# Kernel optimization log

Hardware: AMD Instinct MI355X
Metric: run time of the kernel (lower is better)

## Reference

```python
import jax, jax.numpy as jnp
import numpy as np

T, D, H = 10, 45, 45  # time steps, input features, hidden size (hard-coded in source)


def _lstm_step(x, h, c, W_ih, W_hh, b_ih, b_hh):
    # PyTorch nn.LSTM single step; gate order i, f, g, o
    gates = x @ W_ih.T + b_ih + h @ W_hh.T + b_hh
    i, f, g, o = jnp.split(gates, 4, axis=-1)
    c2 = jax.nn.sigmoid(f) * c + jax.nn.sigmoid(i) * jnp.tanh(g)
    h2 = jax.nn.sigmoid(o) * jnp.tanh(c2)
    return h2, c2


def setup_inputs() -> dict:
    key = jax.random.key(0)
    ks = jax.random.split(key, 20)
    s = 0.1
    return {
        "price_input": jax.random.normal(ks[0], (T, D), dtype=jnp.float32),
        # encoder input attention: Linear(2H+T -> 1)
        "Wa": jax.random.normal(ks[1], (1, 2 * H + T), dtype=jnp.float32) * s,
        "ba": jax.random.normal(ks[2], (1,), dtype=jnp.float32) * s,
        # encoder LSTM
        "Wih_e": jax.random.normal(ks[3], (4 * H, D), dtype=jnp.float32) * s,
        "Whh_e": jax.random.normal(ks[4], (4 * H, H), dtype=jnp.float32) * s,
        "bih_e": jax.random.normal(ks[5], (4 * H,), dtype=jnp.float32) * s,
        "bhh_e": jax.random.normal(ks[6], (4 * H,), dtype=jnp.float32) * s,
        # decoder temporal attention: Linear(2H+D -> D), Tanh, Linear(D -> 1)
        "W1": jax.random.normal(ks[7], (D, 2 * H + D), dtype=jnp.float32) * s,
        "b1": jax.random.normal(ks[8], (D,), dtype=jnp.float32) * s,
        "W2": jax.random.normal(ks[9], (1, D), dtype=jnp.float32) * s,
        "b2": jax.random.normal(ks[10], (1,), dtype=jnp.float32) * s,
        # decoder LSTM (input dim = D)
        "Wih_d": jax.random.normal(ks[11], (4 * H, D), dtype=jnp.float32) * s,
        "Whh_d": jax.random.normal(ks[12], (4 * H, H), dtype=jnp.float32) * s,
        "bih_d": jax.random.normal(ks[13], (4 * H,), dtype=jnp.float32) * s,
        "bhh_d": jax.random.normal(ks[14], (4 * H,), dtype=jnp.float32) * s,
        # final fc: Linear(2H -> predict_size=45)
        "Wfc": jax.random.normal(ks[15], (45, 2 * H), dtype=jnp.float32) * s,
        "bfc": jax.random.normal(ks[16], (45,), dtype=jnp.float32) * s,
    }


def reference(price_input, Wa, ba, Wih_e, Whh_e, bih_e, bhh_e,
              W1, b1, W2, b2, Wih_d, Whh_d, bih_d, bhh_d, Wfc, bfc):
    x = price_input[None]                      # [1, T, D]
    xT = jnp.transpose(x, (0, 2, 1))           # [1, D, T]

    def enc_step(carry, x_t):
        h, c = carry                           # each [1, H]
        hr = jnp.broadcast_to(h[:, None, :], (1, D, H))
        cr = jnp.broadcast_to(c[:, None, :], (1, D, H))
        feat = jnp.concatenate([hr, cr, xT], axis=2)      # [1, D, 2H+T]
        scores = (feat @ Wa.T + ba)[..., 0]               # [1, D]
        attn = jax.nn.softmax(scores, axis=-1)            # over input features
        wi = attn * x_t[None]                             # [1, D]
        h2, c2 = _lstm_step(wi, h, c, Wih_e, Whh_e, bih_e, bhh_e)
        return (h2, c2), h2

    z = jnp.zeros((1, H), dtype=price_input.dtype)
    (_, _), hs = jax.lax.scan(enc_step, (z, z), price_input)
    price_vec = jnp.transpose(hs, (1, 0, 2))              # [1, T, H]

    # decoder: temporal attention over the T encoder states (hidden=cell=0)
    h0 = jnp.zeros((1, H), dtype=price_input.dtype)
    c0 = h0
    hr = jnp.broadcast_to(h0[:, None, :], (1, T, H))
    feat = jnp.concatenate([hr, hr, price_vec], axis=2)   # [1, T, 2H+D]
    scores = (jnp.tanh(feat @ W1.T + b1) @ W2.T + b2)[..., 0]  # [1, T]
    attn = jax.nn.softmax(scores, axis=-1)
    context = jnp.einsum('bt,bth->bh', attn, price_vec)   # [1, H]

    h1, _ = _lstm_step(context, h0, c0, Wih_d, Whh_d, bih_d, bhh_d)
    y_pred = jnp.concatenate([h1, context], axis=1) @ Wfc.T + bfc  # [1, 45]
    return y_pred
```

## Files before the change

kernel.cpp:

```cpp
#include <hip/hip_runtime.h>


static constexpr int NT = 10;
static constexpr int ND = 45;
static constexpr int NH = 45;
static constexpr int NG = 4 * NH;

__device__ __forceinline__ float rcp_(float x) { return __builtin_amdgcn_rcpf(x); }
__device__ __forceinline__ float sigf(float x) { return rcp_(1.0f + __expf(-x)); }
__device__ __forceinline__ float tanh_(float x) { return 1.0f - 2.0f * rcp_(1.0f + __expf(2.0f * x)); }

__global__ __launch_bounds__(256) void darnn_kernel(
    const float* __restrict__ X,
    const float* __restrict__ Wa,
    const float* __restrict__ Wih_e,
    const float* __restrict__ Whh_e,
    const float* __restrict__ bih_e,
    const float* __restrict__ bhh_e,
    const float* __restrict__ W1,
    const float* __restrict__ b1,
    const float* __restrict__ W2,
    const float* __restrict__ Wih_d,
    const float* __restrict__ bih_d,
    const float* __restrict__ bhh_d,
    const float* __restrict__ Wfc,
    const float* __restrict__ bfc,
    float* __restrict__ out)
{
    const int tid  = threadIdx.x;
    const int wave = tid >> 6;
    const int lane = tid & 63;
    const int g    = tid - 64;

    __shared__ float sX[NT * ND];
    __shared__ float sattn[ND];
    __shared__ float sWi[NT * ND];
    __shared__ float sGx[NT * NG];
    __shared__ float shs[NT * NH];
    __shared__ float sW1c[ND * ND];
    __shared__ float sWfc[45 * 2 * NH];
    __shared__ float sb1[ND];
    __shared__ float sW2v[ND];
    __shared__ float sbfcv[45];
    __shared__ float sat[NT];
    __shared__ float sctx[NH];
    __shared__ float sh1v[NH];
    __shared__ float sg[NG];
    __shared__ float sdec[NT * NH];

    float w0[45], w1[45], w2[45], w3[45];
    float we[45], wd[45];
    float be = 0.0f, bd = 0.0f;
    if (wave == 0) {
        const int j = (lane < 45) ? lane : 0;
        const float* r0 = Whh_e + (j)       * NH;
        const float* r1 = Whh_e + (45 + j)  * NH;
        const float* r2 = Whh_e + (90 + j)  * NH;
        const float* r3 = Whh_e + (135 + j) * NH;
#pragma unroll
        for (int k = 0; k < 45; ++k) {
            w0[k] = r0[k]; w1[k] = r1[k]; w2[k] = r2[k]; w3[k] = r3[k];
        }
    } else {
        if (g < NG) {
            const float* wrE = Wih_e + g * ND;
            const float* wrD = Wih_d + g * ND;
#pragma unroll
            for (int d = 0; d < 45; ++d) { we[d] = wrE[d]; wd[d] = wrD[d]; }
            be = bih_e[g] + bhh_e[g];
            bd = bih_d[g] + bhh_d[g];
        }
        if (wave >= 2)
            for (int i = tid - 128; i < NT * ND; i += 128) sX[i] = X[i];
    }
    __syncthreads();

    if (wave == 1) {
        float acc = -1e30f;
        if (lane < ND) {
            acc = 0.0f;
            for (int t = 0; t < NT; ++t) acc += Wa[90 + t] * sX[t * ND + lane];
        }
        float m = acc;
        for (int off = 32; off; off >>= 1) m = fmaxf(m, __shfl_xor(m, off, 64));
        float e = (lane < ND) ? __expf(acc - m) : 0.0f;
        float s = e;
        for (int off = 32; off; off >>= 1) s += __shfl_xor(s, off, 64);
        if (lane < ND) sattn[lane] = e * rcp_(s);
        __builtin_amdgcn_s_waitcnt(0);
        __builtin_amdgcn_wave_barrier();
        for (int i = lane; i < NT * ND; i += 64) sWi[i] = sattn[i % ND] * sX[i];
    }
    __syncthreads();

    if (wave > 0 && g < NG) {
        float acc[NT];
#pragma unroll
        for (int t = 0; t < NT; ++t) acc[t] = be;
        for (int d = 0; d < ND; ++d) {
            const float wv = we[d];
#pragma unroll
            for (int t = 0; t < NT; ++t) acc[t] += wv * sWi[t * ND + d];
        }
#pragma unroll
        for (int t = 0; t < NT; ++t) sGx[t * NG + g] = acc[t];
    }
    __syncthreads();

    if (wave == 0) {
        const int j = (lane < 45) ? lane : 0;
        float h = 0.0f, c = 0.0f;
        for (int t = 0; t < NT; ++t) {
            float a0 = sGx[t * NG + j];
            float a1 = sGx[t * NG + 45 + j];
            float a2 = sGx[t * NG + 90 + j];
            float a3 = sGx[t * NG + 135 + j];
#pragma unroll
            for (int k = 0; k < 45; ++k) {
                const float hk = __shfl(h, k, 64);
                a0 += w0[k] * hk; a1 += w1[k] * hk;
                a2 += w2[k] * hk; a3 += w3[k] * hk;
            }
            c = sigf(a1) * c + sigf(a0) * tanh_(a2);
            h = sigf(a3) * tanh_(c);
            if (lane < 45) shs[t * NH + lane] = h;
        }
    } else {
        const int i0 = tid - 64;
        {
            const float2* s2 = (const float2*)Wfc;
            float2* d2 = (float2*)sWfc;
            for (int i = i0; i < 2025; i += 192) d2[i] = s2[i];
        }
        for (int i = i0; i < ND * ND; i += 192) {
            const int r = i / 45, cc = i - r * 45;
            sW1c[i] = W1[r * 135 + 90 + cc];
        }
        if (i0 < 45) { sb1[i0] = b1[i0]; sW2v[i0] = W2[i0]; sbfcv[i0] = bfc[i0]; }
    }
    __syncthreads();

    for (int i = tid; i < NT * NH; i += 256) {
        const int t = i / NH, k = i - t * NH;
        const float* wr = sW1c + k * ND;
        const float* hv = shs + t * NH;
        float a = sb1[k];
        for (int jj = 0; jj < ND; ++jj) a += wr[jj] * hv[jj];
        sdec[i] = sW2v[k] * tanh_(a);
    }
    __syncthreads();

    if (tid < NT) {
        float a = 0.0f;
        for (int k = 0; k < NH; ++k) a += sdec[tid * NH + k];
        sat[tid] = a;
    }
    __syncthreads();
    if (tid == 0) {
        float m = -1e30f;
        for (int t = 0; t < NT; ++t) m = fmaxf(m, sat[t]);
        float e[NT], s = 0.0f;
        for (int t = 0; t < NT; ++t) { e[t] = __expf(sat[t] - m); s += e[t]; }
        const float inv = rcp_(s);
        for (int t = 0; t < NT; ++t) sat[t] = e[t] * inv;
    }
    __syncthreads();

    if (tid < NH) {
        float a = 0.0f;
        for (int t = 0; t < NT; ++t) a += sat[t] * shs[t * NH + tid];
        sctx[tid] = a;
    }
    __syncthreads();

    if (wave > 0 && g < NG) {
        float a = bd;
#pragma unroll
        for (int d = 0; d < 45; ++d) a += wd[d] * sctx[d];
        sg[g] = a;
    }
    __syncthreads();
    if (tid < NH) {
        const float ig = sigf(sg[tid]);
        const float gg = tanh_(sg[2 * NH + tid]);
        const float og = sigf(sg[3 * NH + tid]);
        sh1v[tid] = og * tanh_(ig * gg);
    }
    __syncthreads();

    if (tid < 45) {
        const float* wr = sWfc + tid * (2 * NH);
        float a = sbfcv[tid];
        for (int jj = 0; jj < NH; ++jj) a += wr[jj] * sh1v[jj];
        for (int jj = 0; jj < NH; ++jj) a += wr[NH + jj] * sctx[jj];
        out[tid] = a;
    }
}

extern "C" void kernel_launch(void* const* d_in, const int* in_sizes, int n_in,
                              void* d_out, int out_size, void* d_ws, size_t ws_size,
                              hipStream_t stream) {
    const float* X     = (const float*)d_in[0];
    const float* Wa    = (const float*)d_in[1];
    const float* Wih_e = (const float*)d_in[3];
    const float* Whh_e = (const float*)d_in[4];
    const float* bih_e = (const float*)d_in[5];
    const float* bhh_e = (const float*)d_in[6];
    const float* W1    = (const float*)d_in[7];
    const float* b1    = (const float*)d_in[8];
    const float* W2    = (const float*)d_in[9];
    const float* Wih_d = (const float*)d_in[11];
    const float* bih_d = (const float*)d_in[13];
    const float* bhh_d = (const float*)d_in[14];
    const float* Wfc   = (const float*)d_in[15];
    const float* bfc   = (const float*)d_in[16];
    float* out = (float*)d_out;

    darnn_kernel<<<dim3(1), dim3(256), 0, stream>>>(
        X, Wa, Wih_e, Whh_e, bih_e, bhh_e, W1, b1, W2,
        Wih_d, bih_d, bhh_d, Wfc, bfc, out);
}
```

Before: 105.6 us.

## Stage recurrent and input weights through shared memory with coalesced float4 loads

Weight loading changes from strided per-thread row reads from global memory to coalesced float4 copies. Whh_e is staged into a shared buffer that the recurrent wave then reads into registers. Wih_e is held in registers as float4s and written into the same buffer after Whh_e is consumed, and later phases reuse that buffer for Wfc and W1. This targets the uncoalesced global load latency at kernel start, which dominates a single-block kernel. The cost is an extra barrier, a shared memory round trip, and higher register pressure from the staged float4 array.

Measured after the change: 108.9 us. 1.03x slower.

```diff
diff --git a/kernel.cpp b/kernel.cpp
--- a/kernel.cpp
+++ b/kernel.cpp
@@ -32,50 +32,73 @@
     const int lane = tid & 63;
     const int g    = tid - 64;
 
+    __shared__ float sR1[8100];
+    __shared__ float sGx[NT * NG];
     __shared__ float sX[NT * ND];
+    __shared__ float sWi[NT * ND];
+    __shared__ float shs[NT * NH];
+    __shared__ float sdec[NT * NH];
     __shared__ float sattn[ND];
-    __shared__ float sWi[NT * ND];
-    __shared__ float sGx[NT * NG];
-    __shared__ float shs[NT * NH];
-    __shared__ float sW1c[ND * ND];
-    __shared__ float sWfc[45 * 2 * NH];
-    __shared__ float sb1[ND];
-    __shared__ float sW2v[ND];
-    __shared__ float sbfcv[45];
     __shared__ float sat[NT];
     __shared__ float sctx[NH];
     __shared__ float sh1v[NH];
     __shared__ float sg[NG];
-    __shared__ float sdec[NT * NH];
+    __shared__ float sb1[ND];
+    __shared__ float sW2v[ND];
+    __shared__ float sbfcv[45];
+
+    float wd[45];
+    float bd = 0.0f, be = 0.0f;
+    float4 re[11];
+
+    {
+        const float4* src = (const float4*)Whh_e;
+        float4*       dst = (float4*)sR1;
+#pragma unroll
+        for (int k = 0; k < 8; ++k) {
+            const int i = tid + k * 256;
+            if (i < 2025) dst[i] = src[i];
+        }
+    }
+    if (wave == 0) {
+        const float2* x2 = (const float2*)X;
+        float2*       d2 = (float2*)sX;
+#pragma unroll
+        for (int k = 0; k < 4; ++k) {
+            const int i = lane + k * 64;
+            if (i < 225) d2[i] = x2[i];
+        }
+    } else {
+        if (g < NG) {
+            const float* wrD = Wih_d + g * ND;
+#pragma unroll
+            for (int d = 0; d < 45; ++d) wd[d] = wrD[d];
+            be = bih_e[g] + bhh_e[g];
+            bd = bih_d[g] + bhh_d[g];
+        }
+        {
+            const float4* src = (const float4*)Wih_e;
+            const int s = tid - 64;
+#pragma unroll
+            for (int k = 0; k < 11; ++k) {
+                const int i = s + k * 192;
+                if (i < 2025) re[k] = src[i];
+            }
+        }
+    }
+    __syncthreads();
 
     float w0[45], w1[45], w2[45], w3[45];
-    float we[45], wd[45];
-    float be = 0.0f, bd = 0.0f;
     if (wave == 0) {
         const int j = (lane < 45) ? lane : 0;
-        const float* r0 = Whh_e + (j)       * NH;
-        const float* r1 = Whh_e + (45 + j)  * NH;
-        const float* r2 = Whh_e + (90 + j)  * NH;
-        const float* r3 = Whh_e + (135 + j) * NH;
 #pragma unroll
         for (int k = 0; k < 45; ++k) {
-            w0[k] = r0[k]; w1[k] = r1[k]; w2[k] = r2[k]; w3[k] = r3[k];
-        }
-    } else {
-        if (g < NG) {
-            const float* wrE = Wih_e + g * ND;
-            const float* wrD = Wih_d + g * ND;
-#pragma unroll
-            for (int d = 0; d < 45; ++d) { we[d] = wrE[d]; wd[d] = wrD[d]; }
-            be = bih_e[g] + bhh_e[g];
-            bd = bih_d[g] + bhh_d[g];
-        }
-        if (wave >= 2)
-            for (int i = tid - 128; i < NT * ND; i += 128) sX[i] = X[i];
-    }
-    __syncthreads();
-
-    if (wave == 1) {
+            w0[k] = sR1[j * 45 + k];
+            w1[k] = sR1[(45 + j) * 45 + k];
+            w2[k] = sR1[(90 + j) * 45 + k];
+            w3[k] = sR1[(135 + j) * 45 + k];
+        }
+    } else if (wave == 1) {
         float acc = -1e30f;
         if (lane < ND) {
             acc = 0.0f;
@@ -93,7 +116,21 @@
     }
     __syncthreads();
 
+    if (wave > 0) {
+        float4* dst = (float4*)sR1;
+        const int s = tid - 64;
+#pragma unroll
+        for (int k = 0; k < 11; ++k) {
+            const int i = s + k * 192;
+            if (i < 2025) dst[i] = re[k];
+        }
+    }
+    __syncthreads();
+
     if (wave > 0 && g < NG) {
+        float we[45];
+#pragma unroll
+        for (int d = 0; d < 45; ++d) we[d] = sR1[g * 45 + d];
         float acc[NT];
 #pragma unroll
         for (int t = 0; t < NT; ++t) acc[t] = be;
@@ -129,12 +166,12 @@
         const int i0 = tid - 64;
         {
             const float2* s2 = (const float2*)Wfc;
-            float2* d2 = (float2*)sWfc;
+            float2* d2 = (float2*)sR1;
             for (int i = i0; i < 2025; i += 192) d2[i] = s2[i];
         }
         for (int i = i0; i < ND * ND; i += 192) {
             const int r = i / 45, cc = i - r * 45;
-            sW1c[i] = W1[r * 135 + 90 + cc];
+            sR1[4050 + i] = W1[r * 135 + 90 + cc];
         }
         if (i0 < 45) { sb1[i0] = b1[i0]; sW2v[i0] = W2[i0]; sbfcv[i0] = bfc[i0]; }
     }
@@ -142,7 +179,7 @@
 
     for (int i = tid; i < NT * NH; i += 256) {
         const int t = i / NH, k = i - t * NH;
-        const float* wr = sW1c + k * ND;
+        const float* wr = sR1 + 4050 + k * ND;
         const float* hv = shs + t * NH;
         float a = sb1[k];
         for (int jj = 0; jj < ND; ++jj) a += wr[jj] * hv[jj];
@@ -189,7 +226,7 @@
     __syncthreads();
 
     if (tid < 45) {
-        const float* wr = sWfc + tid * (2 * NH);
+        const float* wr = sR1 + tid * (2 * NH);
         float a = sbfcv[tid];
         for (int jj = 0; jj < NH; ++jj) a += wr[jj] * sh1v[jj];
         for (int jj = 0; jj < NH; ++jj) a += wr[NH + jj] * sctx[jj];
```
